# Kernel optimization log

Hardware: AMD Instinct MI355X
Metric: run time of the kernel (lower is better)

## Reference

```python
import jax, jax.numpy as jnp
import numpy as np

V, D, H, B, S, K = 10000, 128, 512, 32, 512, 2  # vocab, emb, hidden, batch, seq, num_cells

def setup_inputs() -> dict:
    key = jax.random.key(0)
    ks = jax.random.split(key, 8)
    sc_d, sc_h = 1.0 / np.sqrt(D), 1.0 / np.sqrt(H)
    return {
        "x": jax.random.randint(ks[0], (B, S), 0, V),
        "emb_table": jax.random.normal(ks[1], (V, D), jnp.float32),
        "W_ih": jax.random.uniform(ks[2], (K, 4 * H, D), jnp.float32, -sc_d, sc_d),
        "W_hh": jax.random.uniform(ks[3], (K, 4 * H, H), jnp.float32, -sc_h, sc_h),
        "b_ih": jax.random.uniform(ks[4], (K, 4 * H), jnp.float32, -sc_h, sc_h),
        "b_hh": jax.random.uniform(ks[5], (K, 4 * H), jnp.float32, -sc_h, sc_h),
        "W_out": jax.random.uniform(ks[6], (V, H), jnp.float32, -sc_h, sc_h),
        "b_out": jax.random.uniform(ks[7], (V,), jnp.float32, -sc_h, sc_h),
    }

def _mlstm(x_ids_t, emb_t, W_ih, W_hh, b, h0, c0):
    # x_ids_t: (S,B) int, emb_t: (S,B,D). Two LSTMCells; token id parity picks the cell.
    def step(carry, inp):
        h, c = carry                       # (B,H) each
        xt, ids = inp                      # (B,D), (B,)
        gates = (jnp.einsum('bd,kgd->kbg', xt, W_ih)
                 + jnp.einsum('bh,kgh->kbg', h, W_hh)
                 + b[:, None, :])          # (K,B,4H)
        i, f, g, o = jnp.split(gates, 4, axis=-1)
        i, f, o = jax.nn.sigmoid(i), jax.nn.sigmoid(f), jax.nn.sigmoid(o)
        g = jnp.tanh(g)
        c_new = f * c + i * g              # (K,B,H)
        h_new = o * jnp.tanh(c_new)        # (K,B,H)
        sel = (ids % 2)[:, None]           # (B,1) cell index per example
        h_next = jnp.where(sel == 0, h_new[0], h_new[1])
        c_next = jnp.where(sel == 0, c_new[0], c_new[1])
        return (h_next, c_next), h_next
    (_, _), hs = jax.lax.scan(step, (h0, c0), (emb_t, x_ids_t))
    return hs  # (S,B,H)

def reference(x, emb_table, W_ih, W_hh, b_ih, b_hh, W_out, b_out):
    emb = emb_table[x]                     # (B,S,D)
    emb_t = jnp.transpose(emb, (1, 0, 2))  # (S,B,D) time-major
    h0 = jnp.zeros((x.shape[0], W_hh.shape[-1]), emb.dtype)
    hs = _mlstm(x.T, emb_t, W_ih, W_hh, b_ih + b_hh, h0, h0)  # (S,B,H)
    flat = hs.reshape(-1, hs.shape[-1])    # (S*B, H)
    logits = flat @ W_out.T + b_out        # (S*B, V)
    return jax.nn.log_softmax(logits, axis=1)
```

## Files before the change

### kernel.cpp

```cpp
#include <hip/hip_runtime.h>
#include <hip/hip_bf16.h>

typedef __attribute__((ext_vector_type(8))) short short8;
typedef __attribute__((ext_vector_type(4))) float f32x4;
typedef unsigned long long u64;

#define V_N 10000
#define D_E 128
#define H_N 512
#define B_N 32
#define S_N 512

#define SENT64 0xFFFFFFFFFFFFFFFFull

#define OFF_RP    0
#define OFF_EMB   5242880
#define OFF_HS    (OFF_EMB + 4194304)
#define OFF_WOUT  (OFF_HS + 16777216)

__device__ __forceinline__ float ftanh(float x) {
  float e = __expf(-2.f * fabsf(x));
  float r = (1.f - e) / (1.f + e);
  return __builtin_copysignf(r, x);
}

union U128 { f32x4 f; u64 q[2]; };

__global__ void k_prep_emb(const int* __restrict__ x, const float* __restrict__ tab,
                           __hip_bfloat16* __restrict__ emb) {
  int i = blockIdx.x * 256 + threadIdx.x;
  if (i >= S_N * B_N * D_E) return;
  int d  = i & (D_E - 1);
  int sb = i >> 7;
  int b  = sb & (B_N - 1);
  int s  = sb >> 5;
  int tok = x[b * S_N + s];
  emb[i] = __float2bfloat16(tab[tok * D_E + d]);
}

__global__ void k_prep_wout(const float* __restrict__ w, __hip_bfloat16* __restrict__ o) {
  int i = blockIdx.x * 256 + threadIdx.x;
  if (i < V_N * H_N) o[i] = __float2bfloat16(w[i]);
}

__launch_bounds__(512, 1)
__global__ void k_recurrence(const int* __restrict__ x,
                             const float* __restrict__ W_ih, const float* __restrict__ W_hh,
                             const float* __restrict__ b_ih, const float* __restrict__ b_hh,
                             const __hip_bfloat16* __restrict__ emb,
                             __hip_bfloat16* __restrict__ hs)
{
  __shared__ __align__(16) __hip_bfloat16 Bl[32][648];
  __shared__ float gl[128][34];
  __shared__ float bias[128];
  __shared__ unsigned short hloc[16][32];

  const int tid = threadIdx.x;
  const int wg  = blockIdx.x;
  const int lane = tid & 63, wv = tid >> 6;
  const int lrow = lane & 15, lk = (lane >> 4) * 8;
  const int b_ep = tid & 31, jj_ep = tid >> 5;

  short8 Afrag[20];
  #pragma unroll
  for (int ks = 0; ks < 20; ++ks) {
    int lr = wv * 16 + lrow;
    int q = lr >> 5, kc = (lr >> 4) & 1, jj = lr & 15;
    int grow = kc * 2048 + q * 512 + wg * 16 + jj;
    int c0 = ks * 32 + lk;
    short8 a;
    #pragma unroll
    for (int e = 0; e < 8; ++e) {
      int c = c0 + e;
      float v = (c < 128) ? W_ih[(size_t)grow * 128 + c]
                          : W_hh[(size_t)grow * 512 + (c - 128)];
      __hip_bfloat16 hb = __float2bfloat16(v);
      a[e] = *(const short*)&hb;
    }
    Afrag[ks] = a;
  }
  if (tid < 128) {
    int lr = tid;
    int q = lr >> 5, kc = (lr >> 4) & 1, jj = lr & 15;
    int grow = kc * 2048 + q * 512 + wg * 16 + jj;
    bias[lr] = b_ih[grow] + b_hh[grow];
  }

  unsigned par[16];
  #pragma unroll
  for (int w = 0; w < 16; ++w) {
    unsigned p = 0;
    for (int bb = 0; bb < 32; ++bb)
      p |= (unsigned)(x[b_ep * S_N + w * 32 + bb] & 1) << bb;
    par[w] = p;
  }

  float c_state = 0.f;

  for (int t = 0; t < S_N; ++t) {
    {
      const f32x4* e16 = (const f32x4*)(emb + (size_t)t * B_N * D_E);
      int ex = tid >> 4, col = tid & 15;
      *(f32x4*)((char*)&Bl[0][0] + ex * 1296 + col * 16) = e16[tid];
    }
    if (t == 0) {
      for (int i = tid; i < 4096; i += 512) {
        int b = i >> 7, hh = i & 127;
        *(u64*)&Bl[b][128 + hh * 4] = 0ull;
      }
    } else {
      const char* srcb = (const char*)hs + (size_t)(t - 1) * 32768;
      U128 buf[4];
      unsigned pend = 0xFu;
      while (pend) {
        #pragma unroll
        for (int c = 0; c < 4; ++c)
          if (pend & (1u << c))
            asm volatile("global_load_dwordx4 %0, %1, off sc0 sc1"
                         : "=v"(buf[c].f) : "v"(srcb + (c * 8192 + tid * 16)) : "memory");
        asm volatile("s_waitcnt vmcnt(0)" ::: "memory");
        __builtin_amdgcn_sched_barrier(0);
        #pragma unroll
        for (int c = 0; c < 4; ++c)
          if ((pend & (1u << c)) && buf[c].q[0] != SENT64 && buf[c].q[1] != SENT64) {
            int ci = c * 512 + tid;
            *(f32x4*)((char*)&Bl[0][0] + (ci >> 6) * 1296 + 256 + (ci & 63) * 16) = buf[c].f;
            pend &= ~(1u << c);
          }
      }
    }
    __syncthreads();

    {
      f32x4 acc0 = {0.f,0.f,0.f,0.f}, acc1 = {0.f,0.f,0.f,0.f};
      #pragma unroll
      for (int ks = 0; ks < 20; ++ks) {
        int cb = (ks * 32 + lk) * 2;
        short8 b0 = *(const short8*)((const char*)&Bl[0][0] + lrow * 1296 + cb);
        short8 b1 = *(const short8*)((const char*)&Bl[0][0] + (16 + lrow) * 1296 + cb);
        acc0 = __builtin_amdgcn_mfma_f32_16x16x32_bf16(Afrag[ks], b0, acc0, 0, 0, 0);
        acc1 = __builtin_amdgcn_mfma_f32_16x16x32_bf16(Afrag[ks], b1, acc1, 0, 0, 0);
      }
      int r0 = wv * 16 + (lane >> 4) * 4;
      int cb0 = lane & 15;
      #pragma unroll
      for (int r = 0; r < 4; ++r) {
        gl[r0 + r][cb0]      = acc0[r];
        gl[r0 + r][16 + cb0] = acc1[r];
      }
    }
    __syncthreads();

    {
      float cand_c[2], cand_h[2];
      #pragma unroll
      for (int kc = 0; kc < 2; ++kc) {
        int base = kc * 16 + jj_ep;
        float ig = gl[base][b_ep]      + bias[base];
        float fg = gl[32 + base][b_ep] + bias[32 + base];
        float gg = gl[64 + base][b_ep] + bias[64 + base];
        float og = gl[96 + base][b_ep] + bias[96 + base];
        ig = 1.f / (1.f + __expf(-ig));
        fg = 1.f / (1.f + __expf(-fg));
        og = 1.f / (1.f + __expf(-og));
        gg = ftanh(gg);
        float cn = fg * c_state + ig * gg;
        cand_c[kc] = cn;
        cand_h[kc] = og * ftanh(cn);
      }
      int sel = (par[t >> 5] >> (t & 31)) & 1;
      c_state  = sel ? cand_c[1] : cand_c[0];
      float hv = sel ? cand_h[1] : cand_h[0];
      __hip_bfloat16 hb = __float2bfloat16(hv);
      hloc[jj_ep][b_ep] = *(const unsigned short*)&hb;
    }
    __syncthreads();

    if (tid < 128) {
      int ex = tid >> 2, part = tid & 3;
      u64 v = (u64)hloc[part * 4 + 0][ex]
            | ((u64)hloc[part * 4 + 1][ex] << 16)
            | ((u64)hloc[part * 4 + 2][ex] << 32)
            | ((u64)hloc[part * 4 + 3][ex] << 48);
      u64* dst = (u64*)hs + (size_t)t * 4096 + ex * 128 + wg * 4 + part;
      __hip_atomic_store(dst, v, __ATOMIC_RELAXED, __HIP_MEMORY_SCOPE_AGENT);
    }
  }
}

__launch_bounds__(256, 2)
__global__ void k_gemm(const __hip_bfloat16* __restrict__ hs,
                       const __hip_bfloat16* __restrict__ wout,
                       const float* __restrict__ b_out,
                       float* __restrict__ out,
                       float* __restrict__ rowpart)
{
  __shared__ __hip_bfloat16 Al[128][72];
  __shared__ __hip_bfloat16 Wt[128][72];
  __shared__ float sumLDS[2][128];
  const int tid = threadIdx.x;
  const int tn = blockIdx.x, tm = blockIdx.y;
  const int lane = tid & 63, wv = tid >> 6;
  const int mq = wv & 1, nq = wv >> 1;
  const int lrow = lane & 15, lk = (lane >> 4) * 8;
  f32x4 acc[4][4] = {};

  const int ar = tid >> 3, ac = (tid & 7) * 8;
  for (int k0 = 0; k0 < 512; k0 += 64) {
    __syncthreads();
    #pragma unroll
    for (int rr = 0; rr < 4; ++rr) {
      int r = ar + rr * 32;
      short8 av = *(const short8*)(hs + ((size_t)(tm * 128 + r)) * 512 + k0 + ac);
      *(short8*)&Al[r][ac] = av;
      int v = tn * 128 + r;
      short8 wvv = {};
      if (v < V_N) wvv = *(const short8*)(wout + (size_t)v * 512 + k0 + ac);
      *(short8*)&Wt[r][ac] = wvv;
    }
    __syncthreads();
    #pragma unroll
    for (int ks = 0; ks < 2; ++ks) {
      int kb = ks * 32 + lk;
      short8 af[4], bf[4];
      #pragma unroll
      for (int i = 0; i < 4; ++i) af[i] = *(const short8*)&Al[mq * 64 + i * 16 + lrow][kb];
      #pragma unroll
      for (int i = 0; i < 4; ++i) bf[i] = *(const short8*)&Wt[nq * 64 + i * 16 + lrow][kb];
      #pragma unroll
      for (int i = 0; i < 4; ++i)
        #pragma unroll
        for (int jx = 0; jx < 4; ++jx)
          acc[i][jx] = __builtin_amdgcn_mfma_f32_16x16x32_bf16(af[i], bf[jx], acc[i][jx], 0, 0, 0);
    }
  }
  const int rbase = tm * 128 + mq * 64 + (lane >> 4) * 4;
  const int cbase = tn * 128 + nq * 64 + (lane & 15);
  float esum[4][4];
  #pragma unroll
  for (int i = 0; i < 4; ++i)
    #pragma unroll
    for (int r = 0; r < 4; ++r) esum[i][r] = 0.f;

  #pragma unroll
  for (int i = 0; i < 4; ++i) {
    #pragma unroll
    for (int jx = 0; jx < 4; ++jx) {
      int col = cbase + jx * 16;
      if (col < V_N) {
        float bo = b_out[col];
        #pragma unroll
        for (int r = 0; r < 4; ++r) {
          int row = rbase + i * 16 + r;
          float lg = acc[i][jx][r] + bo;
          __hip_bfloat16* lrow16 =
            (__hip_bfloat16*)((char*)out + (size_t)row * (V_N * 4) + V_N * 2);
          lrow16[col] = __float2bfloat16(lg);
          esum[i][r] += __expf(lg);
        }
      }
    }
  }
  #pragma unroll
  for (int i = 0; i < 4; ++i) {
    #pragma unroll
    for (int r = 0; r < 4; ++r) {
      float s = esum[i][r];
      s += __shfl_xor(s, 1); s += __shfl_xor(s, 2);
      s += __shfl_xor(s, 4); s += __shfl_xor(s, 8);
      if ((lane & 15) == 0)
        sumLDS[nq][mq * 64 + i * 16 + (lane >> 4) * 4 + r] = s;
    }
  }
  __syncthreads();
  if (tid < 128)
    rowpart[(size_t)(tm * 128 + tid) * 80 + tn] = sumLDS[0][tid] + sumLDS[1][tid];
}

__launch_bounds__(256)
__global__ void k_lsm_fix(float* __restrict__ out, const float* __restrict__ rowpart) {
  const int r = blockIdx.x;
  const int tid = threadIdx.x;
  const float* rp = rowpart + (size_t)r * 80;
  float s = 0.f;
  for (int p = 0; p < 79; ++p) s += rp[p];
  float lse = __logf(s);

  const f32x4* src = (const f32x4*)((const char*)out + (size_t)r * (V_N * 4) + V_N * 2);
  U128 c[5];
  #pragma unroll
  for (int i = 0; i < 5; ++i) {
    int idx = tid + i * 256;
    if (idx < 1250) c[i].f = src[idx];
  }
  __syncthreads();
  float* dst = out + (size_t)r * V_N;
  #pragma unroll
  for (int i = 0; i < 5; ++i) {
    int idx = tid + i * 256;
    if (idx < 1250) {
      const unsigned short* u = (const unsigned short*)&c[i];
      float4 lo, hi;
      lo.x = __uint_as_float((unsigned)u[0] << 16) - lse;
      lo.y = __uint_as_float((unsigned)u[1] << 16) - lse;
      lo.z = __uint_as_float((unsigned)u[2] << 16) - lse;
      lo.w = __uint_as_float((unsigned)u[3] << 16) - lse;
      hi.x = __uint_as_float((unsigned)u[4] << 16) - lse;
      hi.y = __uint_as_float((unsigned)u[5] << 16) - lse;
      hi.z = __uint_as_float((unsigned)u[6] << 16) - lse;
      hi.w = __uint_as_float((unsigned)u[7] << 16) - lse;
      *(float4*)(dst + idx * 8)     = lo;
      *(float4*)(dst + idx * 8 + 4) = hi;
    }
  }
}

extern "C" void kernel_launch(void* const* d_in, const int* in_sizes, int n_in,
                              void* d_out, int out_size, void* d_ws, size_t ws_size,
                              hipStream_t stream) {
  const int*   x    = (const int*)d_in[0];
  const float* tab  = (const float*)d_in[1];
  const float* Wih  = (const float*)d_in[2];
  const float* Whh  = (const float*)d_in[3];
  const float* bih  = (const float*)d_in[4];
  const float* bhh  = (const float*)d_in[5];
  const float* Wout = (const float*)d_in[6];
  const float* bout = (const float*)d_in[7];
  float* out = (float*)d_out;

  char* ws = (char*)d_ws;
  float*           rowpart = (float*)(ws + OFF_RP);
  __hip_bfloat16*  emb     = (__hip_bfloat16*)(ws + OFF_EMB);
  __hip_bfloat16*  hsbuf   = (__hip_bfloat16*)(ws + OFF_HS);
  __hip_bfloat16*  wob     = (__hip_bfloat16*)(ws + OFF_WOUT);

  hipMemsetAsync(hsbuf, 0xFF, (size_t)S_N * B_N * H_N * 2, stream);
  k_prep_emb<<<(S_N * B_N * D_E) / 256, 256, 0, stream>>>(x, tab, emb);
  k_prep_wout<<<(V_N * H_N) / 256, 256, 0, stream>>>(Wout, wob);
  k_recurrence<<<32, 512, 0, stream>>>(x, Wih, Whh, bih, bhh, emb, hsbuf);
  k_gemm<<<dim3(79, 128), 256, 0, stream>>>(hsbuf, wob, bout, out, rowpart);
  k_lsm_fix<<<16384, 256, 0, stream>>>(out, rowpart);
}
```

Measured before the change: 2.363 ms.

## Reorder weight rows so LSTM gate epilogue runs directly in MFMA registers

Weight rows loaded into the A fragments are permuted so that each lane's four MFMA accumulator values hold the i, f, g, o gates of one hidden unit and one cell. The pointwise LSTM update then runs straight from registers, and the two cell candidates are exchanged with a cross-lane shuffle. This removes the gates shared-memory buffer, one __syncthreads and the LDS round trip on every serial timestep. In exchange, each thread now computes two batch columns and keeps two parity tables, which adds register pressure and duplicates transcendental work across lanes.

```diff
diff --git a/kernel.cpp b/kernel.cpp
--- a/kernel.cpp
+++ b/kernel.cpp
@@ -51,51 +51,56 @@
                              __hip_bfloat16* __restrict__ hs)
 {
   __shared__ __align__(16) __hip_bfloat16 Bl[32][648];
-  __shared__ float gl[128][34];
-  __shared__ float bias[128];
   __shared__ unsigned short hloc[16][32];
 
   const int tid = threadIdx.x;
   const int wg  = blockIdx.x;
   const int lane = tid & 63, wv = tid >> 6;
   const int lrow = lane & 15, lk = (lane >> 4) * 8;
-  const int b_ep = tid & 31, jj_ep = tid >> 5;
 
   short8 Afrag[20];
-  #pragma unroll
-  for (int ks = 0; ks < 20; ++ks) {
-    int lr = wv * 16 + lrow;
-    int q = lr >> 5, kc = (lr >> 4) & 1, jj = lr & 15;
-    int grow = kc * 2048 + q * 512 + wg * 16 + jj;
-    int c0 = ks * 32 + lk;
-    short8 a;
-    #pragma unroll
-    for (int e = 0; e < 8; ++e) {
-      int c = c0 + e;
-      float v = (c < 128) ? W_ih[(size_t)grow * 128 + c]
-                          : W_hh[(size_t)grow * 512 + (c - 128)];
-      __hip_bfloat16 hb = __float2bfloat16(v);
-      a[e] = *(const short*)&hb;
-    }
-    Afrag[ks] = a;
-  }
-  if (tid < 128) {
-    int lr = tid;
-    int q = lr >> 5, kc = (lr >> 4) & 1, jj = lr & 15;
-    int grow = kc * 2048 + q * 512 + wg * 16 + jj;
-    bias[lr] = b_ih[grow] + b_hh[grow];
-  }
-
-  unsigned par[16];
+  {
+    int kcA = lrow >> 3, jpA = (lrow >> 2) & 1, gateA = lrow & 3;
+    int grow = kcA * 2048 + gateA * 512 + wg * 16 + wv * 2 + jpA;
+    #pragma unroll
+    for (int ks = 0; ks < 20; ++ks) {
+      int c0 = ks * 32 + lk;
+      short8 a;
+      #pragma unroll
+      for (int e = 0; e < 8; ++e) {
+        int c = c0 + e;
+        float v = (c < 128) ? W_ih[(size_t)grow * 128 + c]
+                            : W_hh[(size_t)grow * 512 + (c - 128)];
+        __hip_bfloat16 hb = __float2bfloat16(v);
+        a[e] = *(const short*)&hb;
+      }
+      Afrag[ks] = a;
+    }
+  }
+
+  const int g  = lane >> 4;
+  const int kc = g >> 1, jp = g & 1;
+  const int jj = wv * 2 + jp;
+  float bias4[4];
+  #pragma unroll
+  for (int r = 0; r < 4; ++r) {
+    int gr = kc * 2048 + r * 512 + wg * 16 + jj;
+    bias4[r] = b_ih[gr] + b_hh[gr];
+  }
+
+  const int bA = lane & 15, bB = 16 + bA;
+  unsigned parA[16], parB[16];
   #pragma unroll
   for (int w = 0; w < 16; ++w) {
-    unsigned p = 0;
-    for (int bb = 0; bb < 32; ++bb)
-      p |= (unsigned)(x[b_ep * S_N + w * 32 + bb] & 1) << bb;
-    par[w] = p;
-  }
-
-  float c_state = 0.f;
+    unsigned pa = 0, pb = 0;
+    for (int bb = 0; bb < 32; ++bb) {
+      pa |= (unsigned)(x[bA * S_N + w * 32 + bb] & 1) << bb;
+      pb |= (unsigned)(x[bB * S_N + w * 32 + bb] & 1) << bb;
+    }
+    parA[w] = pa; parB[w] = pb;
+  }
+
+  float csA = 0.f, csB = 0.f;
 
   for (int t = 0; t < S_N; ++t) {
     {
@@ -131,48 +136,50 @@
     }
     __syncthreads();
 
+    f32x4 acc0 = {0.f,0.f,0.f,0.f}, acc1 = {0.f,0.f,0.f,0.f};
+    #pragma unroll
+    for (int ks = 0; ks < 20; ++ks) {
+      int cb = (ks * 32 + lk) * 2;
+      short8 b0 = *(const short8*)((const char*)&Bl[0][0] + lrow * 1296 + cb);
+      short8 b1 = *(const short8*)((const char*)&Bl[0][0] + (16 + lrow) * 1296 + cb);
+      acc0 = __builtin_amdgcn_mfma_f32_16x16x32_bf16(Afrag[ks], b0, acc0, 0, 0, 0);
+      acc1 = __builtin_amdgcn_mfma_f32_16x16x32_bf16(Afrag[ks], b1, acc1, 0, 0, 0);
+    }
+
     {
-      f32x4 acc0 = {0.f,0.f,0.f,0.f}, acc1 = {0.f,0.f,0.f,0.f};
-      #pragma unroll
-      for (int ks = 0; ks < 20; ++ks) {
-        int cb = (ks * 32 + lk) * 2;
-        short8 b0 = *(const short8*)((const char*)&Bl[0][0] + lrow * 1296 + cb);
-        short8 b1 = *(const short8*)((const char*)&Bl[0][0] + (16 + lrow) * 1296 + cb);
-        acc0 = __builtin_amdgcn_mfma_f32_16x16x32_bf16(Afrag[ks], b0, acc0, 0, 0, 0);
-        acc1 = __builtin_amdgcn_mfma_f32_16x16x32_bf16(Afrag[ks], b1, acc1, 0, 0, 0);
-      }
-      int r0 = wv * 16 + (lane >> 4) * 4;
-      int cb0 = lane & 15;
-      #pragma unroll
-      for (int r = 0; r < 4; ++r) {
-        gl[r0 + r][cb0]      = acc0[r];
-        gl[r0 + r][16 + cb0] = acc1[r];
-      }
-    }
-    __syncthreads();
-
-    {
-      float cand_c[2], cand_h[2];
-      #pragma unroll
-      for (int kc = 0; kc < 2; ++kc) {
-        int base = kc * 16 + jj_ep;
-        float ig = gl[base][b_ep]      + bias[base];
-        float fg = gl[32 + base][b_ep] + bias[32 + base];
-        float gg = gl[64 + base][b_ep] + bias[64 + base];
-        float og = gl[96 + base][b_ep] + bias[96 + base];
-        ig = 1.f / (1.f + __expf(-ig));
-        fg = 1.f / (1.f + __expf(-fg));
-        og = 1.f / (1.f + __expf(-og));
-        gg = ftanh(gg);
-        float cn = fg * c_state + ig * gg;
-        cand_c[kc] = cn;
-        cand_h[kc] = og * ftanh(cn);
-      }
-      int sel = (par[t >> 5] >> (t & 31)) & 1;
-      c_state  = sel ? cand_c[1] : cand_c[0];
-      float hv = sel ? cand_h[1] : cand_h[0];
-      __hip_bfloat16 hb = __float2bfloat16(hv);
-      hloc[jj_ep][b_ep] = *(const unsigned short*)&hb;
+      float iA = 1.f / (1.f + __expf(-(acc0[0] + bias4[0])));
+      float fA = 1.f / (1.f + __expf(-(acc0[1] + bias4[1])));
+      float gA = ftanh(acc0[2] + bias4[2]);
+      float oA = 1.f / (1.f + __expf(-(acc0[3] + bias4[3])));
+      float cnA = fA * csA + iA * gA;
+      float hnA = oA * ftanh(cnA);
+
+      float iB = 1.f / (1.f + __expf(-(acc1[0] + bias4[0])));
+      float fB = 1.f / (1.f + __expf(-(acc1[1] + bias4[1])));
+      float gB = ftanh(acc1[2] + bias4[2]);
+      float oB = 1.f / (1.f + __expf(-(acc1[3] + bias4[3])));
+      float cnB = fB * csB + iB * gB;
+      float hnB = oB * ftanh(cnB);
+
+      float pcA = __shfl_xor(cnA, 32), phA = __shfl_xor(hnA, 32);
+      float pcB = __shfl_xor(cnB, 32), phB = __shfl_xor(hnB, 32);
+
+      float c0A = kc ? pcA : cnA, c1A = kc ? cnA : pcA;
+      float h0A = kc ? phA : hnA, h1A = kc ? hnA : phA;
+      float c0B = kc ? pcB : cnB, c1B = kc ? cnB : pcB;
+      float h0B = kc ? phB : hnB, h1B = kc ? hnB : phB;
+
+      int selA = (parA[t >> 5] >> (t & 31)) & 1;
+      int selB = (parB[t >> 5] >> (t & 31)) & 1;
+      csA = selA ? c1A : c0A;  float hA = selA ? h1A : h0A;
+      csB = selB ? c1B : c0B;  float hB = selB ? h1B : h0B;
+
+      if (kc == 0) {
+        __hip_bfloat16 ha = __float2bfloat16(hA);
+        __hip_bfloat16 hb2 = __float2bfloat16(hB);
+        hloc[jj][bA] = *(const unsigned short*)&ha;
+        hloc[jj][bB] = *(const unsigned short*)&hb2;
+      }
     }
     __syncthreads();
 
```

Result: faster. 2.288 ms (-3.2%).
